# Performance work log

Hardware: AMD Instinct MI355X
Metric: run time of the kernel (lower is better)

## Reference

```python
import jax, jax.numpy as jnp
import numpy as np

D_MODEL = 1024

def setup_inputs() -> dict:
    key = jax.random.key(0)
    kx, kq, kk, kv, ko = jax.random.split(key, 5)
    B, S, D = 8, 2048, D_MODEL
    scale = 1.0 / np.sqrt(D)
    x = jax.random.normal(kx, (B, S, D), dtype=jnp.float32)
    # nn.Linear weights are [out, in]; y = x @ W.T
    Wq = jax.random.normal(kq, (D, D), dtype=jnp.float32) * scale
    Wk = jax.random.normal(kk, (D, D), dtype=jnp.float32) * scale
    Wv = jax.random.normal(kv, (D, D), dtype=jnp.float32) * scale
    Wo = jax.random.normal(ko, (D, D), dtype=jnp.float32) * scale
    return {"x": x, "Wq": Wq, "Wk": Wk, "Wv": Wv, "Wo": Wo}

def reference(x, Wq, Wk, Wv, Wo):
    # Single-head self-attention, dropout in eval mode (identity).
    d_model = x.shape[-1]
    q = jnp.einsum('bsd,ed->bse', x, Wq)
    k = jnp.einsum('bsd,ed->bse', x, Wk)
    v = jnp.einsum('bsd,ed->bse', x, Wv)
    scores = jnp.einsum('bqe,bke->bqk', q, k) / jnp.sqrt(jnp.float32(d_model))
    attn = jax.nn.softmax(scores, axis=-1)
    weighted = jnp.einsum('bqk,bke->bqe', attn, v)
    return jnp.einsum('bqe,oe->bqo', weighted, Wo)
```

## Files before the change

kernel.cpp:

```cpp
#include <hip/hip_runtime.h>
#include <hip/hip_bf16.h>
#include <stdint.h>

typedef short bf16x8 __attribute__((ext_vector_type(8)));
typedef float f32x4 __attribute__((ext_vector_type(4)));

__device__ __forceinline__ unsigned short f2bf(float x) {
  uint32_t u = __builtin_bit_cast(uint32_t, x);
  u += 0x7FFFu + ((u >> 16) & 1u);
  return (unsigned short)(u >> 16);
}
__device__ __forceinline__ float bf2f(unsigned short u) {
  uint32_t v = ((uint32_t)u) << 16;
  return __builtin_bit_cast(float, v);
}

__device__ __forceinline__ void gl2lds16(const void* g, void* l) {
  __builtin_amdgcn_global_load_lds(
      (const __attribute__((address_space(1))) unsigned int*)g,
      (__attribute__((address_space(3))) unsigned int*)l, 16, 0, 0);
}

__global__ __launch_bounds__(256) void cast_f32_bf16_k(
    const float* __restrict__ s, unsigned short* __restrict__ d, long n) {
  long i = ((long)blockIdx.x * 256 + threadIdx.x) * 8;
  if (i >= n) return;
  float4 a = *(const float4*)(s + i);
  float4 b = *(const float4*)(s + i + 4);
  bf16x8 o;
  o[0] = (short)f2bf(a.x); o[1] = (short)f2bf(a.y);
  o[2] = (short)f2bf(a.z); o[3] = (short)f2bf(a.w);
  o[4] = (short)f2bf(b.x); o[5] = (short)f2bf(b.y);
  o[6] = (short)f2bf(b.z); o[7] = (short)f2bf(b.w);
  *(bf16x8*)(d + i) = o;
}

__global__ __launch_bounds__(256) void cast4_f32_bf16_k(
    const float* __restrict__ s0, const float* __restrict__ s1,
    const float* __restrict__ s2, const float* __restrict__ s3,
    unsigned short* __restrict__ d, long n) {
  const float* s = blockIdx.z == 0 ? s0 : blockIdx.z == 1 ? s1 : blockIdx.z == 2 ? s2 : s3;
  long i = ((long)blockIdx.x * 256 + threadIdx.x) * 8;
  if (i >= n) return;
  float4 a = *(const float4*)(s + i);
  float4 b = *(const float4*)(s + i + 4);
  bf16x8 o;
  o[0] = (short)f2bf(a.x); o[1] = (short)f2bf(a.y);
  o[2] = (short)f2bf(a.z); o[3] = (short)f2bf(a.w);
  o[4] = (short)f2bf(b.x); o[5] = (short)f2bf(b.y);
  o[6] = (short)f2bf(b.z); o[7] = (short)f2bf(b.w);
  *(bf16x8*)(d + blockIdx.z * n + i) = o;
}

template <typename OutT, bool TRANSV>
__global__ __launch_bounds__(512, 2) void gemm_bt8(
    const unsigned short* __restrict__ A, const unsigned short* __restrict__ B,
    OutT* __restrict__ C, int M, int N, int K,
    long sA, long sB, long sC, float alpha) {
  extern __shared__ __align__(16) char smem[];
  const int bz = blockIdx.z;
  const int gx = gridDim.x;
  const int nwg = gx * gridDim.y;
  const int idx = blockIdx.y * gx + blockIdx.x;
  const int wg = (idx & 7) * (nwg >> 3) + (idx >> 3);
  const int bm = wg / gx, bn = wg % gx;

  const int tid = threadIdx.x, lane = tid & 63, wave = tid >> 6;
  const int wm = wave >> 2, wn = wave & 3;

  const char* Ac = (const char*)(A + (long)bz * sA + (long)bm * 256 * K);
  const char* Bc = (const char*)(B + (long)bz * sB + (long)bn * 256 * K);
  C += (long)bz * sC;
  const long ld = (long)K * 2;

  const int sr = tid >> 3;
  const int scol = (((tid & 7) ^ ((tid >> 3) & 7)) << 4);

  auto stageChunk = [&](int buf, int op, int c, const char* gbase, int ktb) {
    char* reg = smem + ((buf * 2 + op) << 15);
    gl2lds16(gbase + (long)(sr + c * 64) * ld + (ktb + scol),
             reg + c * 8192 + tid * 16);
  };

  const int colx0 = ((lane >> 4) << 4) ^ ((lane & 7) << 4);
  const int colx1 = (64 | ((lane >> 4) << 4)) ^ ((lane & 7) << 4);
  const int rbA = (wm * 128 + (lane & 15)) * 128;
  const int rbB = (wn * 64 + (lane & 15)) * 128;

#pragma unroll
  for (int c = 0; c < 4; ++c) stageChunk(0, 0, c, Ac, 0);
#pragma unroll
  for (int c = 0; c < 4; ++c) stageChunk(0, 1, c, Bc, 0);
  asm volatile("s_waitcnt vmcnt(0)" ::: "memory");
  __builtin_amdgcn_s_barrier();
  __builtin_amdgcn_sched_barrier(0);

  f32x4 acc[8][4] = {};
  bf16x8 bfr[4];
  const int nt = K >> 6;
  for (int t = 0; t < nt; ++t) {
    const int b = t & 1;
    const int ktb = (t + 1 < nt ? t + 1 : 0) << 7;
#pragma unroll
    for (int ph = 0; ph < 4; ++ph) {
      const int g = ph & 1, kh = ph >> 1;
      const int colx = kh ? colx1 : colx0;
      stageChunk(b ^ 1, ph >> 1, (ph & 1) * 2 + 0, (ph >> 1) ? Bc : Ac, ktb);
      stageChunk(b ^ 1, ph >> 1, (ph & 1) * 2 + 1, (ph >> 1) ? Bc : Ac, ktb);
      const char* regA = smem + ((b * 2 + 0) << 15);
      const char* regB = smem + ((b * 2 + 1) << 15);
      bf16x8 afr[4];
#pragma unroll
      for (int m = 0; m < 4; ++m)
        afr[m] = *(const bf16x8*)(regA + rbA + g * (64 * 128) + m * (16 * 128) + colx);
      if (g == 0) {
#pragma unroll
        for (int n = 0; n < 4; ++n)
          bfr[n] = *(const bf16x8*)(regB + rbB + n * (16 * 128) + colx);
      }
      __builtin_amdgcn_s_barrier();
      asm volatile("s_waitcnt lgkmcnt(0)" ::: "memory");
      __builtin_amdgcn_sched_barrier(0);
      __builtin_amdgcn_s_setprio(1);
#pragma unroll
      for (int m = 0; m < 4; ++m)
#pragma unroll
        for (int n = 0; n < 4; ++n)
          acc[g * 4 + m][n] = __builtin_amdgcn_mfma_f32_16x16x32_bf16(
              afr[m], bfr[n], acc[g * 4 + m][n], 0, 0, 0);
      __builtin_amdgcn_s_setprio(0);
      if (ph == 3) asm volatile("s_waitcnt vmcnt(0)" ::: "memory");
      __builtin_amdgcn_s_barrier();
      __builtin_amdgcn_sched_barrier(0);
    }
  }

  const long row0 = (long)bm * 256 + wm * 128 + (lane >> 4) * 4;
  const int col0 = bn * 256 + wn * 64 + (lane & 15);
#pragma unroll
  for (int m = 0; m < 8; ++m) {
#pragma unroll
    for (int n = 0; n < 4; ++n) {
      if constexpr (TRANSV) {
        long row = row0 + m * 16;
        long base = ((row >> 11) << 21) + ((long)(col0 + n * 16) << 11) + (row & 2047);
        ushort4 st;
        st.x = f2bf(acc[m][n][0]); st.y = f2bf(acc[m][n][1]);
        st.z = f2bf(acc[m][n][2]); st.w = f2bf(acc[m][n][3]);
        *(ushort4*)((unsigned short*)C + base) = st;
      } else {
#pragma unroll
        for (int r = 0; r < 4; ++r) {
          long row = row0 + m * 16 + r;
          int col = col0 + n * 16;
          float v = acc[m][n][r] * alpha;
          if constexpr (sizeof(OutT) == 2)
            C[row * (long)N + col] = (OutT)f2bf(v);
          else
            C[row * (long)N + col] = v;
        }
      }
    }
  }
}

__global__ __launch_bounds__(256) void softmax_inplace(unsigned short* __restrict__ s, int C) {
  __shared__ float red[8];
  long row = blockIdx.x;
  unsigned short* p = s + row * (long)C;
  int tid = threadIdx.x, lane = tid & 63, w = tid >> 6;
  bf16x8 raw = *(const bf16x8*)(p + tid * 8);
  float v[8];
  float mx = -3.4e38f;
#pragma unroll
  for (int j = 0; j < 8; ++j) { v[j] = bf2f((unsigned short)raw[j]); mx = fmaxf(mx, v[j]); }
#pragma unroll
  for (int o = 32; o > 0; o >>= 1) mx = fmaxf(mx, __shfl_xor(mx, o));
  if (lane == 0) red[w] = mx;
  __syncthreads();
  mx = fmaxf(fmaxf(red[0], red[1]), fmaxf(red[2], red[3]));
  float sum = 0.f;
#pragma unroll
  for (int j = 0; j < 8; ++j) { v[j] = __expf(v[j] - mx); sum += v[j]; }
#pragma unroll
  for (int o = 32; o > 0; o >>= 1) sum += __shfl_xor(sum, o);
  if (lane == 0) red[4 + w] = sum;
  __syncthreads();
  float inv = 1.f / (red[4] + red[5] + red[6] + red[7]);
  bf16x8 o8;
#pragma unroll
  for (int j = 0; j < 8; ++j) o8[j] = (short)f2bf(v[j] * inv);
  *(bf16x8*)(p + tid * 8) = o8;
}

extern "C" void kernel_launch(void* const* d_in, const int* in_sizes, int n_in,
                              void* d_out, int out_size, void* d_ws, size_t ws_size,
                              hipStream_t stream) {
  (void)in_sizes; (void)n_in; (void)out_size; (void)ws_size;
  const float* x  = (const float*)d_in[0];
  const float* Wq = (const float*)d_in[1];
  const float* Wk = (const float*)d_in[2];
  const float* Wv = (const float*)d_in[3];
  const float* Wo = (const float*)d_in[4];
  const int B = 8, S = 2048, D = 1024;
  const long MB = 1 << 20;
  char* w = (char*)d_ws;
  unsigned short* Wqb = (unsigned short*)(w + 0 * MB);
  unsigned short* Wkb = (unsigned short*)(w + 2 * MB);
  unsigned short* Wvb = (unsigned short*)(w + 4 * MB);
  unsigned short* Wob = (unsigned short*)(w + 6 * MB);
  unsigned short* xb  = (unsigned short*)(w + 8 * MB);
  unsigned short* qb  = (unsigned short*)(w + 40 * MB);
  unsigned short* kb  = (unsigned short*)(w + 72 * MB);
  unsigned short* vt  = (unsigned short*)(w + 104 * MB);
  unsigned short* wb  = xb;
  unsigned short* attn = (unsigned short*)d_out;
  float* out = (float*)d_out;

  long nx = (long)B * S * D;
  long nw = (long)D * D;

  const int LDSB = 131072;
  hipFuncSetAttribute((const void*)gemm_bt8<unsigned short, false>,
                      hipFuncAttributeMaxDynamicSharedMemorySize, LDSB);
  hipFuncSetAttribute((const void*)gemm_bt8<unsigned short, true>,
                      hipFuncAttributeMaxDynamicSharedMemorySize, LDSB);
  hipFuncSetAttribute((const void*)gemm_bt8<float, false>,
                      hipFuncAttributeMaxDynamicSharedMemorySize, LDSB);

  cast_f32_bf16_k<<<(int)(nx / 2048), 256, 0, stream>>>(x, xb, nx);
  dim3 gW((int)(nw / 2048), 1, 4);
  cast4_f32_bf16_k<<<gW, 256, 0, stream>>>(Wq, Wk, Wv, Wo, Wqb, nw);

  dim3 gP(D / 256, (B * S) / 256, 1);
  gemm_bt8<unsigned short, false><<<gP, 512, LDSB, stream>>>(xb, Wqb, qb, B * S, D, D, 0, 0, 0, 1.f);
  gemm_bt8<unsigned short, false><<<gP, 512, LDSB, stream>>>(xb, Wkb, kb, B * S, D, D, 0, 0, 0, 1.f);
  gemm_bt8<unsigned short, true><<<gP, 512, LDSB, stream>>>(xb, Wvb, vt, B * S, D, D, 0, 0, 0, 1.f);

  dim3 gS(S / 256, S / 256, B);
  gemm_bt8<unsigned short, false><<<gS, 512, LDSB, stream>>>(qb, kb, attn, S, S, D,
      (long)S * D, (long)S * D, (long)S * S, 0.03125f);

  softmax_inplace<<<B * S, 256, 0, stream>>>(attn, S);

  dim3 gPV(D / 256, S / 256, B);
  gemm_bt8<unsigned short, false><<<gPV, 512, LDSB, stream>>>(attn, vt, wb, S, D, S,
      (long)S * S, (long)D * S, (long)S * D, 1.f);

  gemm_bt8<float, false><<<gP, 512, LDSB, stream>>>(wb, Wob, out, B * S, D, D, 0, 0, 0, 1.f);
}
```

Measured before the change: 346.5 us.

## Fuse QKV projections into one GEMM and software-pipeline LDS fragment reads

Replaces the three separate Q/K/V projection GEMMs with one N=3072 GEMM over the contiguous bf16 weight buffers. Its epilogue routes column blocks to q, k, or transposed v outputs. The GEMM main loop is restructured to double-buffer A/B register fragments, issuing LDS reads for the next sub-step before the current MFMAs, with partial lgkmcnt waits. This aims to cut launch overhead, improve tile scheduling, and hide LDS latency behind MFMA, at the cost of more registers and more fragile wait counts.

```diff
diff --git a/kernel.cpp b/kernel.cpp
--- a/kernel.cpp
+++ b/kernel.cpp
@@ -52,7 +52,7 @@
   *(bf16x8*)(d + blockIdx.z * n + i) = o;
 }
 
-template <typename OutT, bool TRANSV>
+template <typename OutT, bool FUSEQKV>
 __global__ __launch_bounds__(512, 2) void gemm_bt8(
     const unsigned short* __restrict__ A, const unsigned short* __restrict__ B,
     OutT* __restrict__ C, int M, int N, int K,
@@ -87,68 +87,120 @@
   const int rbA = (wm * 128 + (lane & 15)) * 128;
   const int rbB = (wn * 64 + (lane & 15)) * 128;
 
+  f32x4 acc[8][4] = {};
+  bf16x8 a0[4], a1[4], b0[4], b1[4];
+
+  auto rdA = [&](bf16x8* dst, const char* reg, int g, int colx) {
+#pragma unroll
+    for (int m = 0; m < 4; ++m)
+      dst[m] = *(const bf16x8*)(reg + rbA + g * (64 * 128) + m * (16 * 128) + colx);
+  };
+  auto rdB = [&](bf16x8* dst, const char* reg, int colx) {
+#pragma unroll
+    for (int n = 0; n < 4; ++n)
+      dst[n] = *(const bf16x8*)(reg + rbB + n * (16 * 128) + colx);
+  };
+  auto mfma16 = [&](const bf16x8* af, const bf16x8* bf_, int g) {
+    __builtin_amdgcn_s_setprio(1);
+#pragma unroll
+    for (int m = 0; m < 4; ++m)
+#pragma unroll
+      for (int n = 0; n < 4; ++n)
+        acc[g * 4 + m][n] = __builtin_amdgcn_mfma_f32_16x16x32_bf16(
+            af[m], bf_[n], acc[g * 4 + m][n], 0, 0, 0);
+    __builtin_amdgcn_s_setprio(0);
+    __builtin_amdgcn_sched_barrier(0);
+  };
+
 #pragma unroll
   for (int c = 0; c < 4; ++c) stageChunk(0, 0, c, Ac, 0);
 #pragma unroll
   for (int c = 0; c < 4; ++c) stageChunk(0, 1, c, Bc, 0);
   asm volatile("s_waitcnt vmcnt(0)" ::: "memory");
   __builtin_amdgcn_s_barrier();
-  __builtin_amdgcn_sched_barrier(0);
-
-  f32x4 acc[8][4] = {};
-  bf16x8 bfr[4];
+  rdA(a0, smem, 0, colx0);
+  rdB(b0, smem + (1 << 15), colx0);
+
   const int nt = K >> 6;
   for (int t = 0; t < nt; ++t) {
     const int b = t & 1;
-    const int ktb = (t + 1 < nt ? t + 1 : 0) << 7;
-#pragma unroll
-    for (int ph = 0; ph < 4; ++ph) {
-      const int g = ph & 1, kh = ph >> 1;
-      const int colx = kh ? colx1 : colx0;
-      stageChunk(b ^ 1, ph >> 1, (ph & 1) * 2 + 0, (ph >> 1) ? Bc : Ac, ktb);
-      stageChunk(b ^ 1, ph >> 1, (ph & 1) * 2 + 1, (ph >> 1) ? Bc : Ac, ktb);
-      const char* regA = smem + ((b * 2 + 0) << 15);
-      const char* regB = smem + ((b * 2 + 1) << 15);
-      bf16x8 afr[4];
-#pragma unroll
-      for (int m = 0; m < 4; ++m)
-        afr[m] = *(const bf16x8*)(regA + rbA + g * (64 * 128) + m * (16 * 128) + colx);
-      if (g == 0) {
-#pragma unroll
-        for (int n = 0; n < 4; ++n)
-          bfr[n] = *(const bf16x8*)(regB + rbB + n * (16 * 128) + colx);
-      }
+    const bool pf = (t + 1 < nt);
+    const int ktb = (t + 1) << 7;
+    const char* regA0 = smem + ((b * 2 + 0) << 15);
+    const char* regB0 = smem + ((b * 2 + 1) << 15);
+    const char* regA1 = smem + (((b ^ 1) * 2 + 0) << 15);
+    const char* regB1 = smem + (((b ^ 1) * 2 + 1) << 15);
+
+    if (pf) {
+#pragma unroll
+      for (int c = 0; c < 4; ++c) stageChunk(b ^ 1, 0, c, Ac, ktb);
+    }
+    rdA(a1, regA0, 1, colx0);
+    asm volatile("s_waitcnt lgkmcnt(4)" ::: "memory");
+    __builtin_amdgcn_sched_barrier(0);
+    mfma16(a0, b0, 0);
+    __builtin_amdgcn_s_barrier();
+
+    if (pf) {
+#pragma unroll
+      for (int c = 0; c < 4; ++c) stageChunk(b ^ 1, 1, c, Bc, ktb);
+    }
+    rdA(a0, regA0, 0, colx1);
+    rdB(b1, regB0, colx1);
+    asm volatile("s_waitcnt lgkmcnt(8)" ::: "memory");
+    __builtin_amdgcn_sched_barrier(0);
+    mfma16(a1, b0, 1);
+    __builtin_amdgcn_s_barrier();
+
+    rdA(a1, regA0, 1, colx1);
+    asm volatile("s_waitcnt lgkmcnt(4)" ::: "memory");
+    __builtin_amdgcn_sched_barrier(0);
+    mfma16(a0, b1, 0);
+    __builtin_amdgcn_s_barrier();
+
+    if (pf) {
+      asm volatile("s_waitcnt vmcnt(0)" ::: "memory");
       __builtin_amdgcn_s_barrier();
+      rdA(a0, regA1, 0, colx0);
+      rdB(b0, regB1, colx0);
+      asm volatile("s_waitcnt lgkmcnt(8)" ::: "memory");
+    } else {
       asm volatile("s_waitcnt lgkmcnt(0)" ::: "memory");
-      __builtin_amdgcn_sched_barrier(0);
-      __builtin_amdgcn_s_setprio(1);
-#pragma unroll
-      for (int m = 0; m < 4; ++m)
-#pragma unroll
-        for (int n = 0; n < 4; ++n)
-          acc[g * 4 + m][n] = __builtin_amdgcn_mfma_f32_16x16x32_bf16(
-              afr[m], bfr[n], acc[g * 4 + m][n], 0, 0, 0);
-      __builtin_amdgcn_s_setprio(0);
-      if (ph == 3) asm volatile("s_waitcnt vmcnt(0)" ::: "memory");
-      __builtin_amdgcn_s_barrier();
-      __builtin_amdgcn_sched_barrier(0);
-    }
+    }
+    __builtin_amdgcn_sched_barrier(0);
+    mfma16(a1, b1, 1);
+    __builtin_amdgcn_s_barrier();
   }
 
   const long row0 = (long)bm * 256 + wm * 128 + (lane >> 4) * 4;
   const int col0 = bn * 256 + wn * 64 + (lane & 15);
-#pragma unroll
-  for (int m = 0; m < 8; ++m) {
-#pragma unroll
-    for (int n = 0; n < 4; ++n) {
-      if constexpr (TRANSV) {
-        long row = row0 + m * 16;
-        long base = ((row >> 11) << 21) + ((long)(col0 + n * 16) << 11) + (row & 2047);
-        ushort4 st;
-        st.x = f2bf(acc[m][n][0]); st.y = f2bf(acc[m][n][1]);
-        st.z = f2bf(acc[m][n][2]); st.w = f2bf(acc[m][n][3]);
-        *(ushort4*)((unsigned short*)C + base) = st;
-      } else {
+  if constexpr (FUSEQKV) {
+    const int tensor = bn >> 2;
+    unsigned short* dst = (unsigned short*)C + ((long)tensor << 24);
+    const int colb0 = col0 - (tensor << 10);
+#pragma unroll
+    for (int m = 0; m < 8; ++m) {
+#pragma unroll
+      for (int n = 0; n < 4; ++n) {
+        if (tensor < 2) {
+#pragma unroll
+          for (int r = 0; r < 4; ++r)
+            dst[(row0 + m * 16 + r) * 1024 + colb0 + n * 16] = f2bf(acc[m][n][r]);
+        } else {
+          long row = row0 + m * 16;
+          long base = ((row >> 11) << 21) + ((long)(colb0 + n * 16) << 11) + (row & 2047);
+          ushort4 st;
+          st.x = f2bf(acc[m][n][0]); st.y = f2bf(acc[m][n][1]);
+          st.z = f2bf(acc[m][n][2]); st.w = f2bf(acc[m][n][3]);
+          *(ushort4*)(dst + base) = st;
+        }
+      }
+    }
+  } else {
+#pragma unroll
+    for (int m = 0; m < 8; ++m) {
+#pragma unroll
+      for (int n = 0; n < 4; ++n) {
 #pragma unroll
         for (int r = 0; r < 4; ++r) {
           long row = row0 + m * 16 + r;
@@ -206,8 +258,6 @@
   const long MB = 1 << 20;
   char* w = (char*)d_ws;
   unsigned short* Wqb = (unsigned short*)(w + 0 * MB);
-  unsigned short* Wkb = (unsigned short*)(w + 2 * MB);
-  unsigned short* Wvb = (unsigned short*)(w + 4 * MB);
   unsigned short* Wob = (unsigned short*)(w + 6 * MB);
   unsigned short* xb  = (unsigned short*)(w + 8 * MB);
   unsigned short* qb  = (unsigned short*)(w + 40 * MB);
@@ -221,9 +271,9 @@
   long nw = (long)D * D;
 
   const int LDSB = 131072;
+  hipFuncSetAttribute((const void*)gemm_bt8<unsigned short, true>,
+                      hipFuncAttributeMaxDynamicSharedMemorySize, LDSB);
   hipFuncSetAttribute((const void*)gemm_bt8<unsigned short, false>,
-                      hipFuncAttributeMaxDynamicSharedMemorySize, LDSB);
-  hipFuncSetAttribute((const void*)gemm_bt8<unsigned short, true>,
                       hipFuncAttributeMaxDynamicSharedMemorySize, LDSB);
   hipFuncSetAttribute((const void*)gemm_bt8<float, false>,
                       hipFuncAttributeMaxDynamicSharedMemorySize, LDSB);
@@ -232,10 +282,9 @@
   dim3 gW((int)(nw / 2048), 1, 4);
   cast4_f32_bf16_k<<<gW, 256, 0, stream>>>(Wq, Wk, Wv, Wo, Wqb, nw);
 
-  dim3 gP(D / 256, (B * S) / 256, 1);
-  gemm_bt8<unsigned short, false><<<gP, 512, LDSB, stream>>>(xb, Wqb, qb, B * S, D, D, 0, 0, 0, 1.f);
-  gemm_bt8<unsigned short, false><<<gP, 512, LDSB, stream>>>(xb, Wkb, kb, B * S, D, D, 0, 0, 0, 1.f);
-  gemm_bt8<unsigned short, true><<<gP, 512, LDSB, stream>>>(xb, Wvb, vt, B * S, D, D, 0, 0, 0, 1.f);
+  dim3 gF(3072 / 256, (B * S) / 256, 1);
+  gemm_bt8<unsigned short, true><<<gF, 512, LDSB, stream>>>(
+      xb, Wqb, qb, B * S, 3072, D, 0, 0, 0, 1.f);
 
   dim3 gS(S / 256, S / 256, B);
   gemm_bt8<unsigned short, false><<<gS, 512, LDSB, stream>>>(qb, kb, attn, S, S, D,
@@ -247,5 +296,6 @@
   gemm_bt8<unsigned short, false><<<gPV, 512, LDSB, stream>>>(attn, vt, wb, S, D, S,
       (long)S * S, (long)D * S, (long)S * D, 1.f);
 
+  dim3 gP(D / 256, (B * S) / 256, 1);
   gemm_bt8<float, false><<<gP, 512, LDSB, stream>>>(wb, Wob, out, B * S, D, D, 0, 0, 0, 1.f);
 }
```

Result: faster. 324.4 us (-6.4%).
